# Kernel tuning notes

Hardware: AMD Instinct MI355X
Metric: run time of the kernel (lower is better)

Reference implementation:

```python
import jax, jax.numpy as jnp
import numpy as np

B, H, KVH, HD, S = 16, 32, 8, 128, 4096
D = H * HD  # 4096
Q = 1  # decode: one query token per batch element


def rotate_half(x):
    half = x.shape[-1] // 2
    return jnp.concatenate([-x[..., half:], x[..., :half]], axis=-1)


def setup_inputs() -> dict:
    key = jax.random.key(0)
    ks = jax.random.split(key, 8)
    hidden_states = jax.random.normal(ks[0], (B, Q, D), dtype=jnp.float32)
    current_steps = jax.random.randint(ks[1], (B,), 0, S - 1)
    # additive causal mask per batch: positions <= current_step visible
    pos = jnp.arange(S)[None, :]
    attention_mask = jnp.where(pos <= current_steps[:, None], 0.0, -1e9).astype(jnp.float32)[:, None, None, :]  # [B,1,1,S]
    # RoPE cos/sin at each batch element's current position
    inv_freq = 1.0 / (10000.0 ** (jnp.arange(0, HD, 2, dtype=jnp.float32) / HD))
    ang = current_steps[:, None].astype(jnp.float32) * inv_freq[None, :]  # [B, HD/2]
    ang = jnp.concatenate([ang, ang], axis=-1)  # [B, HD]
    cos = jnp.cos(ang)[:, None, None, :]  # [B,1,1,HD]
    sin = jnp.sin(ang)[:, None, None, :]
    past_key = jax.random.normal(ks[2], (B, KVH, S, HD), dtype=jnp.float32)
    past_value = jax.random.normal(ks[3], (B, KVH, S, HD), dtype=jnp.float32)
    sc = 1.0 / np.sqrt(D)
    Wq = jax.random.normal(ks[4], (D, H * HD), dtype=jnp.float32) * sc
    Wk = jax.random.normal(ks[5], (D, KVH * HD), dtype=jnp.float32) * sc
    Wv = jax.random.normal(ks[6], (D, KVH * HD), dtype=jnp.float32) * sc
    Wo = jax.random.normal(ks[7], (H * HD, D), dtype=jnp.float32) * sc
    return dict(hidden_states=hidden_states, attention_mask=attention_mask,
                current_steps=current_steps, cos=cos, sin=sin,
                past_key=past_key, past_value=past_value,
                Wq=Wq, Wk=Wk, Wv=Wv, Wo=Wo)


def reference(hidden_states, attention_mask, current_steps, cos, sin,
              past_key, past_value, Wq, Wk, Wv, Wo):
    b, q_len, d = hidden_states.shape
    # projections -> [B, heads, Q, HD]
    q = (hidden_states @ Wq).reshape(b, q_len, H, HD).transpose(0, 2, 1, 3)
    k = (hidden_states @ Wk).reshape(b, q_len, KVH, HD).transpose(0, 2, 1, 3)
    v = (hidden_states @ Wv).reshape(b, q_len, KVH, HD).transpose(0, 2, 1, 3)
    # RoPE
    q = q * cos + rotate_half(q) * sin
    k = k * cos + rotate_half(k) * sin
    # KV-cache scatter at current_step per batch (slice_scatter equivalent)
    def upd(cache_b, new_b, step):
        return jax.lax.dynamic_update_slice(cache_b, new_b, (0, step, 0))
    new_key = jax.vmap(upd)(past_key, k, current_steps)      # [B,KVH,S,HD]
    new_value = jax.vmap(upd)(past_value, v, current_steps)  # [B,KVH,S,HD]
    # GQA attention
    g = H // KVH
    qg = q.reshape(b, KVH, g, q_len, HD)
    scores = jnp.einsum('bkgqd,bksd->bkgqs', qg, new_key) / np.sqrt(HD)
    scores = scores + attention_mask[:, :, None, :, :]  # [B,1,1,Q,S] broadcast
    probs = jax.nn.softmax(scores, axis=-1)
    out = jnp.einsum('bkgqs,bksd->bkgqd', probs, new_value)
    out = out.reshape(b, H, q_len, HD).transpose(0, 2, 1, 3).reshape(b, q_len, H * HD)
    attn_out = out @ Wo
    return attn_out, new_key, new_value
```

## Files before the change

kernel.cpp:

```cpp
#include <hip/hip_runtime.h>

#define B 16
#define H 32
#define KVH 8
#define HD 128
#define S 4096
#define D 4096
#define NQKV 6144
#define PSPLIT 32
#define WSPLIT 32
#define NCH 16
#define CROWS (S / NCH)
#define SCALE 0.08838834764831845f

typedef float nfloat4 __attribute__((ext_vector_type(4)));

__device__ __forceinline__ float4 ntload4(const float4* p) {
  nfloat4 r = __builtin_nontemporal_load(reinterpret_cast<const nfloat4*>(p));
  return *reinterpret_cast<float4*>(&r);
}
__device__ __forceinline__ void ntstore4(float4* p, float4 v) {
  __builtin_nontemporal_store(*reinterpret_cast<nfloat4*>(&v),
                              reinterpret_cast<nfloat4*>(p));
}

__global__ void k_proj(const float* __restrict__ hs, const float* __restrict__ Wq,
                       const float* __restrict__ Wk, const float* __restrict__ Wv,
                       float* __restrict__ part) {
  int n = blockIdx.x * 256 + threadIdx.x;
  int k0 = blockIdx.y * (D / PSPLIT);
  const float* w; int ldw, col;
  if (n < 4096)      { w = Wq; ldw = 4096; col = n; }
  else if (n < 5120) { w = Wk; ldw = 1024; col = n - 4096; }
  else               { w = Wv; ldw = 1024; col = n - 5120; }
  float acc[B];
#pragma unroll
  for (int b = 0; b < B; b++) acc[b] = 0.f;
  const float* wp = w + (size_t)k0 * ldw + col;
#pragma unroll 8
  for (int k = 0; k < D / PSPLIT; k++) {
    float wv = wp[(size_t)k * ldw];
#pragma unroll
    for (int b = 0; b < B; b++) acc[b] = fmaf(hs[b * D + k0 + k], wv, acc[b]);
  }
  float* p = part + (size_t)blockIdx.y * (B * NQKV);
#pragma unroll
  for (int b = 0; b < B; b++) p[(size_t)b * NQKV + n] = acc[b];
}

__global__ void k_reduce_rope(const float* __restrict__ part, const float* __restrict__ cosb,
                              const float* __restrict__ sinb, const int* __restrict__ steps,
                              float* __restrict__ qr, float* __restrict__ nkrow,
                              float* __restrict__ nvrow) {
  int i = blockIdx.x * 256 + threadIdx.x;
  int b = i / 3584, n2 = i % 3584;
  if (n2 < 2560) {
    int hr = n2 >> 6, d = n2 & 63;
    int n_lo = hr * 128 + d, n_hi = n_lo + 64;
    float vlo = 0.f, vhi = 0.f;
#pragma unroll
    for (int c = 0; c < PSPLIT; c++) {
      const float* pc = part + (size_t)c * B * NQKV + (size_t)b * NQKV;
      vlo += pc[n_lo];
      vhi += pc[n_hi];
    }
    float clo = cosb[b * HD + d], chi = cosb[b * HD + d + 64];
    float slo = sinb[b * HD + d], shi = sinb[b * HD + d + 64];
    float rlo = vlo * clo - vhi * slo;
    float rhi = vhi * chi + vlo * shi;
    if (n_lo < 4096) {
      qr[(size_t)b * D + n_lo] = rlo;
      qr[(size_t)b * D + n_hi] = rhi;
    } else {
      nkrow[(size_t)b * KVH * HD + (n_lo - 4096)] = rlo;
      nkrow[(size_t)b * KVH * HD + (n_hi - 4096)] = rhi;
    }
  } else {
    int j = n2 - 2560;
    float v = 0.f;
#pragma unroll
    for (int c = 0; c < PSPLIT; c++)
      v += part[(size_t)c * B * NQKV + (size_t)b * NQKV + 5120 + j];
    nvrow[(size_t)b * KVH * HD + j] = v;
  }
}

__global__ void k_flashKV(const float* __restrict__ pastk, const float* __restrict__ pastv,
                          const float* __restrict__ nkrow, const float* __restrict__ nvrow,
                          const float* __restrict__ qr, const int* __restrict__ steps,
                          float* __restrict__ newk, float* __restrict__ newv,
                          float* __restrict__ part, float* __restrict__ stats) {
  int ch = blockIdx.x, kvh = blockIdx.y, b = blockIdx.z;
  int t = threadIdx.x;
  __shared__ float sbuf[CROWS][4];
  __shared__ float redm[4][4];
  __shared__ float4 red4[4][4][32];
  int s0 = ch * CROWS;
  int step = steps[b];
  int L = step + 1;
  int h0 = kvh * 4;
  bool any = (s0 < L);
  int w = t >> 6;

  {
    int ln = t & 15, rg = t >> 4;
    const float4* qbase = (const float4*)(qr + ((size_t)b * H + h0) * HD);
    float4 q0[4], q1[4];
#pragma unroll
    for (int h = 0; h < 4; h++) {
      q0[h] = qbase[h * 32 + ln];
      q1[h] = qbase[h * 32 + ln + 16];
    }
    const float4* subp = (const float4*)(nkrow + (size_t)(b * KVH + kvh) * HD);
    float4 sub0 = subp[ln], sub1 = subp[ln + 16];
    const float4* src = (const float4*)(pastk + ((size_t)(b * KVH + kvh) * S + s0) * HD);
    float4*       dst = (float4*)(newk + ((size_t)(b * KVH + kvh) * S + s0) * HD);
#pragma unroll 4
    for (int it = 0; it < CROWS / 16; ++it) {
      int row = it * 16 + rg;
      size_t o0 = (size_t)row * 32 + ln;
      float4 k0 = ntload4(&src[o0]);
      float4 k1 = ntload4(&src[o0 + 16]);
      if (s0 + row == step) { k0 = sub0; k1 = sub1; }
      ntstore4(&dst[o0], k0);
      ntstore4(&dst[o0 + 16], k1);
      if (s0 + it * 16 < L) {
        float a0, a1, a2, a3;
        a0 = fmaf(k0.x, q0[0].x, fmaf(k0.y, q0[0].y, fmaf(k0.z, q0[0].z, fmaf(k0.w, q0[0].w,
             fmaf(k1.x, q1[0].x, fmaf(k1.y, q1[0].y, fmaf(k1.z, q1[0].z, k1.w * q1[0].w)))))));
        a1 = fmaf(k0.x, q0[1].x, fmaf(k0.y, q0[1].y, fmaf(k0.z, q0[1].z, fmaf(k0.w, q0[1].w,
             fmaf(k1.x, q1[1].x, fmaf(k1.y, q1[1].y, fmaf(k1.z, q1[1].z, k1.w * q1[1].w)))))));
        a2 = fmaf(k0.x, q0[2].x, fmaf(k0.y, q0[2].y, fmaf(k0.z, q0[2].z, fmaf(k0.w, q0[2].w,
             fmaf(k1.x, q1[2].x, fmaf(k1.y, q1[2].y, fmaf(k1.z, q1[2].z, k1.w * q1[2].w)))))));
        a3 = fmaf(k0.x, q0[3].x, fmaf(k0.y, q0[3].y, fmaf(k0.z, q0[3].z, fmaf(k0.w, q0[3].w,
             fmaf(k1.x, q1[3].x, fmaf(k1.y, q1[3].y, fmaf(k1.z, q1[3].z, k1.w * q1[3].w)))))));
#pragma unroll
        for (int o = 1; o < 16; o <<= 1) {
          a0 += __shfl_xor(a0, o);
          a1 += __shfl_xor(a1, o);
          a2 += __shfl_xor(a2, o);
          a3 += __shfl_xor(a3, o);
        }
        if (ln < 4) {
          float my = (ln == 0) ? a0 : (ln == 1) ? a1 : (ln == 2) ? a2 : a3;
          sbuf[row][ln] = my * SCALE;
        }
      }
    }
  }
  __syncthreads();

  bool valid = any && (s0 + t < L);
  float s_0 = valid ? sbuf[t][0] : -1e30f;
  float s_1 = valid ? sbuf[t][1] : -1e30f;
  float s_2 = valid ? sbuf[t][2] : -1e30f;
  float s_3 = valid ? sbuf[t][3] : -1e30f;
  float mx0 = s_0, mx1 = s_1, mx2 = s_2, mx3 = s_3;
#pragma unroll
  for (int o = 1; o < 64; o <<= 1) {
    mx0 = fmaxf(mx0, __shfl_xor(mx0, o));
    mx1 = fmaxf(mx1, __shfl_xor(mx1, o));
    mx2 = fmaxf(mx2, __shfl_xor(mx2, o));
    mx3 = fmaxf(mx3, __shfl_xor(mx3, o));
  }
  if ((t & 63) == 0) { redm[w][0] = mx0; redm[w][1] = mx1; redm[w][2] = mx2; redm[w][3] = mx3; }
  __syncthreads();
  float m0 = fmaxf(fmaxf(redm[0][0], redm[1][0]), fmaxf(redm[2][0], redm[3][0]));
  float m1 = fmaxf(fmaxf(redm[0][1], redm[1][1]), fmaxf(redm[2][1], redm[3][1]));
  float m2 = fmaxf(fmaxf(redm[0][2], redm[1][2]), fmaxf(redm[2][2], redm[3][2]));
  float m3 = fmaxf(fmaxf(redm[0][3], redm[1][3]), fmaxf(redm[2][3], redm[3][3]));
  float e0 = valid ? __expf(s_0 - m0) : 0.f;
  float e1 = valid ? __expf(s_1 - m1) : 0.f;
  float e2 = valid ? __expf(s_2 - m2) : 0.f;
  float e3 = valid ? __expf(s_3 - m3) : 0.f;
  float es0 = e0, es1 = e1, es2 = e2, es3 = e3;
#pragma unroll
  for (int o = 1; o < 64; o <<= 1) {
    es0 += __shfl_xor(es0, o);
    es1 += __shfl_xor(es1, o);
    es2 += __shfl_xor(es2, o);
    es3 += __shfl_xor(es3, o);
  }
  __syncthreads();
  if ((t & 63) == 0) { redm[w][0] = es0; redm[w][1] = es1; redm[w][2] = es2; redm[w][3] = es3; }
  sbuf[t][0] = e0; sbuf[t][1] = e1; sbuf[t][2] = e2; sbuf[t][3] = e3;
  __syncthreads();
  float l0 = redm[0][0] + redm[1][0] + redm[2][0] + redm[3][0];
  float l1 = redm[0][1] + redm[1][1] + redm[2][1] + redm[3][1];
  float l2 = redm[0][2] + redm[1][2] + redm[2][2] + redm[3][2];
  float l3 = redm[0][3] + redm[1][3] + redm[2][3] + redm[3][3];

  int d4 = t & 31, rr = t >> 5;
  float4 a0 = make_float4(0.f, 0.f, 0.f, 0.f), a1 = a0, a2 = a0, a3 = a0;
  {
    float4 vsub = ((const float4*)(nvrow + (size_t)(b * KVH + kvh) * HD))[d4];
    const float4* src = (const float4*)(pastv + ((size_t)(b * KVH + kvh) * S + s0) * HD);
    float4*       dst = (float4*)(newv + ((size_t)(b * KVH + kvh) * S + s0) * HD);
#pragma unroll 4
    for (int i = 0; i < CROWS / 8; ++i) {
      int r = i * 8 + rr;
      float4 v = ntload4(&src[r * 32 + d4]);
      if (s0 + r == step) v = vsub;
      ntstore4(&dst[r * 32 + d4], v);
      if (any && i * 8 < L - s0) {
        float q0 = sbuf[r][0], q1 = sbuf[r][1], q2 = sbuf[r][2], q3 = sbuf[r][3];
        a0.x = fmaf(q0, v.x, a0.x); a0.y = fmaf(q0, v.y, a0.y);
        a0.z = fmaf(q0, v.z, a0.z); a0.w = fmaf(q0, v.w, a0.w);
        a1.x = fmaf(q1, v.x, a1.x); a1.y = fmaf(q1, v.y, a1.y);
        a1.z = fmaf(q1, v.z, a1.z); a1.w = fmaf(q1, v.w, a1.w);
        a2.x = fmaf(q2, v.x, a2.x); a2.y = fmaf(q2, v.y, a2.y);
        a2.z = fmaf(q2, v.z, a2.z); a2.w = fmaf(q2, v.w, a2.w);
        a3.x = fmaf(q3, v.x, a3.x); a3.y = fmaf(q3, v.y, a3.y);
        a3.z = fmaf(q3, v.z, a3.z); a3.w = fmaf(q3, v.w, a3.w);
      }
    }
  }
  a0.x += __shfl_xor(a0.x, 32); a0.y += __shfl_xor(a0.y, 32);
  a0.z += __shfl_xor(a0.z, 32); a0.w += __shfl_xor(a0.w, 32);
  a1.x += __shfl_xor(a1.x, 32); a1.y += __shfl_xor(a1.y, 32);
  a1.z += __shfl_xor(a1.z, 32); a1.w += __shfl_xor(a1.w, 32);
  a2.x += __shfl_xor(a2.x, 32); a2.y += __shfl_xor(a2.y, 32);
  a2.z += __shfl_xor(a2.z, 32); a2.w += __shfl_xor(a2.w, 32);
  a3.x += __shfl_xor(a3.x, 32); a3.y += __shfl_xor(a3.y, 32);
  a3.z += __shfl_xor(a3.z, 32); a3.w += __shfl_xor(a3.w, 32);
  __syncthreads();
  if ((t & 32) == 0) {
    red4[w][0][d4] = a0; red4[w][1][d4] = a1; red4[w][2][d4] = a2; red4[w][3][d4] = a3;
  }
  __syncthreads();
  if (t < 128) {
    int hh = t >> 5, dd = t & 31;
    float4 x0 = red4[0][hh][dd], x1 = red4[1][hh][dd], x2 = red4[2][hh][dd], x3 = red4[3][hh][dd];
    float4 s;
    s.x = (x0.x + x1.x) + (x2.x + x3.x);
    s.y = (x0.y + x1.y) + (x2.y + x3.y);
    s.z = (x0.z + x1.z) + (x2.z + x3.z);
    s.w = (x0.w + x1.w) + (x2.w + x3.w);
    ((float4*)(part + (((size_t)ch * B + b) * KVH + kvh) * 512))[t] = s;
  }
  if (t == 0) {
    size_t si = (((size_t)ch * B + b) * KVH + kvh) * 8;
    stats[si + 0] = m0; stats[si + 1] = l0;
    stats[si + 2] = m1; stats[si + 3] = l1;
    stats[si + 4] = m2; stats[si + 5] = l2;
    stats[si + 6] = m3; stats[si + 7] = l3;
  }
}

__global__ void k_reduce_ctx(const float* __restrict__ part, const float* __restrict__ stats,
                             float* __restrict__ ctx) {
  int i = blockIdx.x * 256 + threadIdx.x;
  int b = i >> 12, r = i & 4095, h = r >> 7, d = r & 127;
  int kvh = h >> 2, hl = h & 3;
  float M = -1e30f;
#pragma unroll
  for (int c = 0; c < NCH; c++)
    M = fmaxf(M, stats[(((size_t)c * B + b) * KVH + kvh) * 8 + hl * 2]);
  float num = 0.f, den = 0.f;
#pragma unroll
  for (int c = 0; c < NCH; c++) {
    size_t si = (((size_t)c * B + b) * KVH + kvh) * 8 + hl * 2;
    float wgt = __expf(stats[si] - M);
    den += wgt * stats[si + 1];
    num += wgt * part[(((size_t)c * B + b) * KVH + kvh) * 512 + hl * 128 + d];
  }
  ctx[i] = num / den;
}

__global__ void k_wo(const float* __restrict__ ctx, const float* __restrict__ Wo,
                     float* __restrict__ part) {
  int n = blockIdx.x * 256 + threadIdx.x;
  int k0 = blockIdx.y * (D / WSPLIT);
  float acc[B];
#pragma unroll
  for (int b = 0; b < B; b++) acc[b] = 0.f;
  const float* wp = Wo + (size_t)k0 * D + n;
#pragma unroll 8
  for (int k = 0; k < D / WSPLIT; k++) {
    float wv = wp[(size_t)k * D];
#pragma unroll
    for (int b = 0; b < B; b++) acc[b] = fmaf(ctx[b * D + k0 + k], wv, acc[b]);
  }
  float* p = part + (size_t)blockIdx.y * (B * D);
#pragma unroll
  for (int b = 0; b < B; b++) p[(size_t)b * D + n] = acc[b];
}

__global__ void k_reduce_out(const float* __restrict__ part, float* __restrict__ out) {
  int i = blockIdx.x * 256 + threadIdx.x;
  float s = 0.f;
#pragma unroll
  for (int c = 0; c < WSPLIT; c++) s += part[(size_t)c * B * D + i];
  out[i] = s;
}

extern "C" void kernel_launch(void* const* d_in, const int* in_sizes, int n_in,
                              void* d_out, int out_size, void* d_ws, size_t ws_size,
                              hipStream_t stream) {
  const float* hs    = (const float*)d_in[0];
  const int*   steps = (const int*)d_in[2];
  const float* cosb  = (const float*)d_in[3];
  const float* sinb  = (const float*)d_in[4];
  const float* pk    = (const float*)d_in[5];
  const float* pvv   = (const float*)d_in[6];
  const float* Wq    = (const float*)d_in[7];
  const float* Wk    = (const float*)d_in[8];
  const float* Wv    = (const float*)d_in[9];
  const float* Wo    = (const float*)d_in[10];

  float* attn_out = (float*)d_out;
  float* newk = attn_out + (size_t)B * D;
  float* newv = newk + (size_t)B * KVH * S * HD;

  float* ws = (float*)d_ws;
  float* A        = ws;
  float* p_part   = A;
  float* p_wopart = A;
  float* p_pvpart = A + 3145728;
  float* p_stats  = p_pvpart + 1048576;
  float* p_qr     = p_stats + 16384;
  float* p_nkrow  = p_qr + (size_t)B * D;
  float* p_nvrow  = p_nkrow + (size_t)B * KVH * HD;
  float* p_ctx    = p_nvrow + (size_t)B * KVH * HD;

  hipLaunchKernelGGL(k_proj, dim3(NQKV / 256, PSPLIT), dim3(256), 0, stream,
                     hs, Wq, Wk, Wv, p_part);
  hipLaunchKernelGGL(k_reduce_rope, dim3(B * 3584 / 256), dim3(256), 0, stream,
                     p_part, cosb, sinb, steps, p_qr, p_nkrow, p_nvrow);
  hipLaunchKernelGGL(k_flashKV, dim3(NCH, KVH, B), dim3(256), 0, stream,
                     pk, pvv, p_nkrow, p_nvrow, p_qr, steps, newk, newv,
                     p_pvpart, p_stats);
  hipLaunchKernelGGL(k_reduce_ctx, dim3(B * D / 256), dim3(256), 0, stream,
                     p_pvpart, p_stats, p_ctx);
  hipLaunchKernelGGL(k_wo, dim3(D / 256, WSPLIT), dim3(256), 0, stream,
                     p_ctx, Wo, p_wopart);
  hipLaunchKernelGGL(k_reduce_out, dim3(B * D / 256), dim3(256), 0, stream,
                     p_wopart, attn_out);
}
```

Measured before the change: 309.0 us.

## Prefetch V rows across softmax phase, trim barriers, use nontemporal weight loads

In the fused attention kernel, the first V-cache rows are now loaded before the softmax reductions and each later pair of rows is register double-buffered, so V memory latency overlaps with softmax and the PV accumulation. Separate shared arrays for the max and sum reductions remove two block barriers. The weight-streaming GEMV loads and the partial-sum reductions now use nontemporal loads to avoid polluting the cache. The prefetch raises register pressure, and __launch_bounds__(256) caps the block size.

Measured after the change: 303.4 us. No clear change (-1.8%).

```diff
diff --git a/kernel.cpp b/kernel.cpp
--- a/kernel.cpp
+++ b/kernel.cpp
@@ -23,6 +23,9 @@
   __builtin_nontemporal_store(*reinterpret_cast<nfloat4*>(&v),
                               reinterpret_cast<nfloat4*>(p));
 }
+__device__ __forceinline__ float ntloadf(const float* p) {
+  return __builtin_nontemporal_load(p);
+}
 
 __global__ void k_proj(const float* __restrict__ hs, const float* __restrict__ Wq,
                        const float* __restrict__ Wk, const float* __restrict__ Wv,
@@ -39,7 +42,7 @@
   const float* wp = w + (size_t)k0 * ldw + col;
 #pragma unroll 8
   for (int k = 0; k < D / PSPLIT; k++) {
-    float wv = wp[(size_t)k * ldw];
+    float wv = ntloadf(&wp[(size_t)k * ldw]);
 #pragma unroll
     for (int b = 0; b < B; b++) acc[b] = fmaf(hs[b * D + k0 + k], wv, acc[b]);
   }
@@ -61,8 +64,8 @@
 #pragma unroll
     for (int c = 0; c < PSPLIT; c++) {
       const float* pc = part + (size_t)c * B * NQKV + (size_t)b * NQKV;
-      vlo += pc[n_lo];
-      vhi += pc[n_hi];
+      vlo += ntloadf(&pc[n_lo]);
+      vhi += ntloadf(&pc[n_hi]);
     }
     float clo = cosb[b * HD + d], chi = cosb[b * HD + d + 64];
     float slo = sinb[b * HD + d], shi = sinb[b * HD + d + 64];
@@ -80,20 +83,22 @@
     float v = 0.f;
 #pragma unroll
     for (int c = 0; c < PSPLIT; c++)
-      v += part[(size_t)c * B * NQKV + (size_t)b * NQKV + 5120 + j];
+      v += ntloadf(&part[(size_t)c * B * NQKV + (size_t)b * NQKV + 5120 + j]);
     nvrow[(size_t)b * KVH * HD + j] = v;
   }
 }
 
-__global__ void k_flashKV(const float* __restrict__ pastk, const float* __restrict__ pastv,
-                          const float* __restrict__ nkrow, const float* __restrict__ nvrow,
-                          const float* __restrict__ qr, const int* __restrict__ steps,
-                          float* __restrict__ newk, float* __restrict__ newv,
-                          float* __restrict__ part, float* __restrict__ stats) {
+__global__ void __launch_bounds__(256)
+k_flashKV(const float* __restrict__ pastk, const float* __restrict__ pastv,
+          const float* __restrict__ nkrow, const float* __restrict__ nvrow,
+          const float* __restrict__ qr, const int* __restrict__ steps,
+          float* __restrict__ newk, float* __restrict__ newv,
+          float* __restrict__ part, float* __restrict__ stats) {
   int ch = blockIdx.x, kvh = blockIdx.y, b = blockIdx.z;
   int t = threadIdx.x;
   __shared__ float sbuf[CROWS][4];
-  __shared__ float redm[4][4];
+  __shared__ float redmx[4][4];
+  __shared__ float redsm[4][4];
   __shared__ float4 red4[4][4][32];
   int s0 = ch * CROWS;
   int step = steps[b];
@@ -101,6 +106,11 @@
   int h0 = kvh * 4;
   bool any = (s0 < L);
   int w = t >> 6;
+  int d4 = t & 31, rr = t >> 5;
+
+  const float4* srcv = (const float4*)(pastv + ((size_t)(b * KVH + kvh) * S + s0) * HD);
+  float4*       dstv = (float4*)(newv + ((size_t)(b * KVH + kvh) * S + s0) * HD);
+  float4 vsub = ((const float4*)(nvrow + (size_t)(b * KVH + kvh) * HD))[d4];
 
   {
     int ln = t & 15, rg = t >> 4;
@@ -148,6 +158,8 @@
       }
     }
   }
+  float4 pv0 = ntload4(&srcv[(size_t)rr * 32 + d4]);
+  float4 pv1 = ntload4(&srcv[(size_t)(rr + 8) * 32 + d4]);
   __syncthreads();
 
   bool valid = any && (s0 + t < L);
@@ -163,12 +175,12 @@
     mx2 = fmaxf(mx2, __shfl_xor(mx2, o));
     mx3 = fmaxf(mx3, __shfl_xor(mx3, o));
   }
-  if ((t & 63) == 0) { redm[w][0] = mx0; redm[w][1] = mx1; redm[w][2] = mx2; redm[w][3] = mx3; }
+  if ((t & 63) == 0) { redmx[w][0] = mx0; redmx[w][1] = mx1; redmx[w][2] = mx2; redmx[w][3] = mx3; }
   __syncthreads();
-  float m0 = fmaxf(fmaxf(redm[0][0], redm[1][0]), fmaxf(redm[2][0], redm[3][0]));
-  float m1 = fmaxf(fmaxf(redm[0][1], redm[1][1]), fmaxf(redm[2][1], redm[3][1]));
-  float m2 = fmaxf(fmaxf(redm[0][2], redm[1][2]), fmaxf(redm[2][2], redm[3][2]));
-  float m3 = fmaxf(fmaxf(redm[0][3], redm[1][3]), fmaxf(redm[2][3], redm[3][3]));
+  float m0 = fmaxf(fmaxf(redmx[0][0], redmx[1][0]), fmaxf(redmx[2][0], redmx[3][0]));
+  float m1 = fmaxf(fmaxf(redmx[0][1], redmx[1][1]), fmaxf(redmx[2][1], redmx[3][1]));
+  float m2 = fmaxf(fmaxf(redmx[0][2], redmx[1][2]), fmaxf(redmx[2][2], redmx[3][2]));
+  float m3 = fmaxf(fmaxf(redmx[0][3], redmx[1][3]), fmaxf(redmx[2][3], redmx[3][3]));
   float e0 = valid ? __expf(s_0 - m0) : 0.f;
   float e1 = valid ? __expf(s_1 - m1) : 0.f;
   float e2 = valid ? __expf(s_2 - m2) : 0.f;
@@ -181,38 +193,46 @@
     es2 += __shfl_xor(es2, o);
     es3 += __shfl_xor(es3, o);
   }
-  __syncthreads();
-  if ((t & 63) == 0) { redm[w][0] = es0; redm[w][1] = es1; redm[w][2] = es2; redm[w][3] = es3; }
+  if ((t & 63) == 0) { redsm[w][0] = es0; redsm[w][1] = es1; redsm[w][2] = es2; redsm[w][3] = es3; }
   sbuf[t][0] = e0; sbuf[t][1] = e1; sbuf[t][2] = e2; sbuf[t][3] = e3;
   __syncthreads();
-  float l0 = redm[0][0] + redm[1][0] + redm[2][0] + redm[3][0];
-  float l1 = redm[0][1] + redm[1][1] + redm[2][1] + redm[3][1];
-  float l2 = redm[0][2] + redm[1][2] + redm[2][2] + redm[3][2];
-  float l3 = redm[0][3] + redm[1][3] + redm[2][3] + redm[3][3];
-
-  int d4 = t & 31, rr = t >> 5;
+  float l0 = redsm[0][0] + redsm[1][0] + redsm[2][0] + redsm[3][0];
+  float l1 = redsm[0][1] + redsm[1][1] + redsm[2][1] + redsm[3][1];
+  float l2 = redsm[0][2] + redsm[1][2] + redsm[2][2] + redsm[3][2];
+  float l3 = redsm[0][3] + redsm[1][3] + redsm[2][3] + redsm[3][3];
+
   float4 a0 = make_float4(0.f, 0.f, 0.f, 0.f), a1 = a0, a2 = a0, a3 = a0;
-  {
-    float4 vsub = ((const float4*)(nvrow + (size_t)(b * KVH + kvh) * HD))[d4];
-    const float4* src = (const float4*)(pastv + ((size_t)(b * KVH + kvh) * S + s0) * HD);
-    float4*       dst = (float4*)(newv + ((size_t)(b * KVH + kvh) * S + s0) * HD);
-#pragma unroll 4
-    for (int i = 0; i < CROWS / 8; ++i) {
-      int r = i * 8 + rr;
-      float4 v = ntload4(&src[r * 32 + d4]);
-      if (s0 + r == step) v = vsub;
-      ntstore4(&dst[r * 32 + d4], v);
-      if (any && i * 8 < L - s0) {
-        float q0 = sbuf[r][0], q1 = sbuf[r][1], q2 = sbuf[r][2], q3 = sbuf[r][3];
-        a0.x = fmaf(q0, v.x, a0.x); a0.y = fmaf(q0, v.y, a0.y);
-        a0.z = fmaf(q0, v.z, a0.z); a0.w = fmaf(q0, v.w, a0.w);
-        a1.x = fmaf(q1, v.x, a1.x); a1.y = fmaf(q1, v.y, a1.y);
-        a1.z = fmaf(q1, v.z, a1.z); a1.w = fmaf(q1, v.w, a1.w);
-        a2.x = fmaf(q2, v.x, a2.x); a2.y = fmaf(q2, v.y, a2.y);
-        a2.z = fmaf(q2, v.z, a2.z); a2.w = fmaf(q2, v.w, a2.w);
-        a3.x = fmaf(q3, v.x, a3.x); a3.y = fmaf(q3, v.y, a3.y);
-        a3.z = fmaf(q3, v.z, a3.z); a3.w = fmaf(q3, v.w, a3.w);
-      }
+#pragma unroll 2
+  for (int i = 0; i < CROWS / 16; ++i) {
+    int r0 = i * 16 + rr, r1 = r0 + 8;
+    float4 v0 = pv0, v1 = pv1;
+    if (i + 1 < CROWS / 16) {
+      pv0 = ntload4(&srcv[(size_t)(r0 + 16) * 32 + d4]);
+      pv1 = ntload4(&srcv[(size_t)(r1 + 16) * 32 + d4]);
+    }
+    if (s0 + r0 == step) v0 = vsub;
+    if (s0 + r1 == step) v1 = vsub;
+    ntstore4(&dstv[(size_t)r0 * 32 + d4], v0);
+    ntstore4(&dstv[(size_t)r1 * 32 + d4], v1);
+    if (any && i * 16 < L - s0) {
+      float p00 = sbuf[r0][0], p01 = sbuf[r0][1], p02 = sbuf[r0][2], p03 = sbuf[r0][3];
+      float p10 = sbuf[r1][0], p11 = sbuf[r1][1], p12 = sbuf[r1][2], p13 = sbuf[r1][3];
+      a0.x = fmaf(p00, v0.x, fmaf(p10, v1.x, a0.x));
+      a0.y = fmaf(p00, v0.y, fmaf(p10, v1.y, a0.y));
+      a0.z = fmaf(p00, v0.z, fmaf(p10, v1.z, a0.z));
+      a0.w = fmaf(p00, v0.w, fmaf(p10, v1.w, a0.w));
+      a1.x = fmaf(p01, v0.x, fmaf(p11, v1.x, a1.x));
+      a1.y = fmaf(p01, v0.y, fmaf(p11, v1.y, a1.y));
+      a1.z = fmaf(p01, v0.z, fmaf(p11, v1.z, a1.z));
+      a1.w = fmaf(p01, v0.w, fmaf(p11, v1.w, a1.w));
+      a2.x = fmaf(p02, v0.x, fmaf(p12, v1.x, a2.x));
+      a2.y = fmaf(p02, v0.y, fmaf(p12, v1.y, a2.y));
+      a2.z = fmaf(p02, v0.z, fmaf(p12, v1.z, a2.z));
+      a2.w = fmaf(p02, v0.w, fmaf(p12, v1.w, a2.w));
+      a3.x = fmaf(p03, v0.x, fmaf(p13, v1.x, a3.x));
+      a3.y = fmaf(p03, v0.y, fmaf(p13, v1.y, a3.y));
+      a3.z = fmaf(p03, v0.z, fmaf(p13, v1.z, a3.z));
+      a3.w = fmaf(p03, v0.w, fmaf(p13, v1.w, a3.w));
     }
   }
   a0.x += __shfl_xor(a0.x, 32); a0.y += __shfl_xor(a0.y, 32);
@@ -223,7 +243,6 @@
   a2.z += __shfl_xor(a2.z, 32); a2.w += __shfl_xor(a2.w, 32);
   a3.x += __shfl_xor(a3.x, 32); a3.y += __shfl_xor(a3.y, 32);
   a3.z += __shfl_xor(a3.z, 32); a3.w += __shfl_xor(a3.w, 32);
-  __syncthreads();
   if ((t & 32) == 0) {
     red4[w][0][d4] = a0; red4[w][1][d4] = a1; red4[w][2][d4] = a2; red4[w][3][d4] = a3;
   }
@@ -277,7 +296,7 @@
   const float* wp = Wo + (size_t)k0 * D + n;
 #pragma unroll 8
   for (int k = 0; k < D / WSPLIT; k++) {
-    float wv = wp[(size_t)k * D];
+    float wv = ntloadf(&wp[(size_t)k * D]);
 #pragma unroll
     for (int b = 0; b < B; b++) acc[b] = fmaf(ctx[b * D + k0 + k], wv, acc[b]);
   }
```
